# Kernel optimization log

Measured on AMD Instinct MI355X. Metric: run time of the kernel, lower is better.

Reference implementation:

```python
import jax, jax.numpy as jnp
import numpy as np

EPS = 1e-5

def _proj(x, w, b, gamma, beta, mean, var):
    # 1x1 conv (einsum over channels) + BatchNorm (inference) ; Dropout is identity in eval.
    y = jnp.einsum('bchw,oc->bohw', x, w) + b[None, :, None, None]
    scale = gamma * jax.lax.rsqrt(var + EPS)
    shift = beta - mean * scale
    return y * scale[None, :, None, None] + shift[None, :, None, None]

def _make_layer(key, cin, cout):
    k1, k2, k3, k4 = jax.random.split(key, 4)
    w = jax.random.normal(k1, (cout, cin), jnp.float32) * (1.0 / np.sqrt(cin))
    b = jax.random.normal(k2, (cout,), jnp.float32) * 0.01
    gamma = 1.0 + 0.1 * jax.random.normal(k3, (cout,), jnp.float32)
    beta = 0.1 * jax.random.normal(k4, (cout,), jnp.float32)
    mean = 0.05 * jax.random.normal(jax.random.fold_in(k1, 7), (cout,), jnp.float32)
    var = 0.5 + jax.random.uniform(jax.random.fold_in(k2, 7), (cout,), jnp.float32)
    return w, b, gamma, beta, mean, var

def setup_inputs() -> dict:
    key = jax.random.key(0)
    B, C, Ci, H, W = 4, 128, 64, 64, 64
    ks = jax.random.split(key, 6)
    inp = {
        'x1': jax.random.normal(ks[0], (B, C, H, W), jnp.float32),
        'x2': jax.random.normal(ks[1], (B, C, H, W), jnp.float32),
    }
    for name, k, cin, cout in [('theta', ks[2], C, Ci), ('phi', ks[3], C, Ci),
                               ('g', ks[4], C, Ci), ('wout', ks[5], Ci, C)]:
        w, b, gm, bt, mn, vr = _make_layer(k, cin, cout)
        inp.update({f'{name}_w': w, f'{name}_b': b, f'{name}_g': gm,
                    f'{name}_beta': bt, f'{name}_m': mn, f'{name}_v': vr})
    return inp

def reference(x1, x2,
              theta_w, theta_b, theta_g, theta_beta, theta_m, theta_v,
              phi_w, phi_b, phi_g, phi_beta, phi_m, phi_v,
              g_w, g_b, g_g, g_beta, g_m, g_v,
              wout_w, wout_b, wout_g, wout_beta, wout_m, wout_v):
    B, C, H, W = x1.shape
    N = H * W
    theta_x1 = _proj(x1, theta_w, theta_b, theta_g, theta_beta, theta_m, theta_v).reshape(B, -1, N)  # [B,Ci,N]
    phi_x2 = _proj(x2, phi_w, phi_b, phi_g, phi_beta, phi_m, phi_v).reshape(B, -1, N)                # [B,Ci,N]
    g_x2 = _proj(x2, g_w, g_b, g_g, g_beta, g_m, g_v).reshape(B, -1, N)                              # [B,Ci,N]
    # attention_map[b, n, m] = sum_c theta[b,c,n] * phi[b,c,m]
    attn = jax.nn.softmax(jnp.einsum('bcn,bcm->bnm', theta_x1, phi_x2), axis=-1)  # [B,N,N]
    out = jnp.einsum('bnm,bcm->bcn', attn, g_x2).reshape(B, -1, H, W)             # [B,Ci,H,W]
    out = _proj(out, wout_w, wout_b, wout_g, wout_beta, wout_m, wout_v)           # [B,C,H,W]
    return jnp.concatenate((out, x1), axis=1)                                     # [B,2C,H,W]
```

## Files before the change

### kernel.cpp

```cpp
#include <hip/hip_runtime.h>
#include <stdint.h>
#include <stddef.h>

#define EPS   1e-5f
#define CINCH 128
#define CI    64
#define NPIX  4096
#define KSPL  4
#define LOG2E 1.44269504088896340736f

typedef __bf16 bf16_t;
typedef _Float16 f16_t;
typedef bf16_t bf16x8 __attribute__((ext_vector_type(8)));
typedef f16_t  f16x8  __attribute__((ext_vector_type(8)));
typedef float  f32x4  __attribute__((ext_vector_type(4)));

typedef __attribute__((address_space(3))) unsigned int lds_u32;
typedef __attribute__((address_space(1))) const unsigned int glb_u32;

__device__ __forceinline__ f32x4 mfma16(bf16x8 a, bf16x8 b, f32x4 c) {
  return __builtin_amdgcn_mfma_f32_16x16x32_bf16(a, b, c, 0, 0, 0);
}
__device__ __forceinline__ f32x4 fzero4() {
  f32x4 z = {0.f, 0.f, 0.f, 0.f};
  return z;
}
__device__ __forceinline__ void gload16(const void* g, void* l) {
  __builtin_amdgcn_global_load_lds((glb_u32*)g, (lds_u32*)l, 16, 0, 0);
}


__global__ __launch_bounds__(256) void proj_all(
    const float* __restrict__ x1, const float* __restrict__ x2,
    const float* __restrict__ tw, const float* __restrict__ tb,
    const float* __restrict__ tg, const float* __restrict__ tbt,
    const float* __restrict__ tm, const float* __restrict__ tv,
    const float* __restrict__ pw, const float* __restrict__ pb,
    const float* __restrict__ pg, const float* __restrict__ pbt,
    const float* __restrict__ pm, const float* __restrict__ pv,
    const float* __restrict__ gw, const float* __restrict__ gb,
    const float* __restrict__ gg, const float* __restrict__ gbt,
    const float* __restrict__ gmn, const float* __restrict__ gv,
    bf16_t* __restrict__ thetaT_h, bf16_t* __restrict__ thetaT_l,
    bf16_t* __restrict__ phiT_h,   bf16_t* __restrict__ phiT_l,
    bf16_t* __restrict__ g_cm,     float* __restrict__ out)
{
  __shared__ float wT[CINCH][CI];
  __shared__ float bf[CI];
  __shared__ float xs[CINCH][32];
  __shared__ __align__(16) char tbuf[32 * 68 * 4];
  float (*tF)[68] = (float(*)[68])tbuf;
  float (*gT)[33] = (float(*)[33])tbuf;

  const int tid = threadIdx.x;
  const int b   = blockIdx.y;
  const int n0  = blockIdx.x * 32;
  const int px  = tid & 31;
  const int og  = tid >> 5;

  auto loadW = [&](const float* w, const float* bb_, const float* gm_,
                   const float* bt_, const float* mn_, const float* vr_,
                   float mul) {
    for (int idx = tid; idx < CI * CINCH; idx += 256) {
      const int o = idx & 63, c = idx >> 6;
      const float sc = gm_[o] * rsqrtf(vr_[o] + EPS);
      wT[c][o] = w[o * CINCH + c] * sc * mul;
      if (c == 0) bf[o] = (bb_[o] * sc + bt_[o] - mn_[o] * sc) * mul;
    }
  };
  auto stageX = [&](const float* x) {
    const float* xsrc = x + (size_t)b * CINCH * NPIX + n0;
#pragma unroll
    for (int i = 0; i < 4; ++i) {
      const int idx = i * 256 + tid;
      const int c = idx >> 3, p = idx & 7;
      *(f32x4*)&xs[c][p * 4] = *(const f32x4*)(xsrc + (size_t)c * NPIX + p * 4);
    }
  };
  auto compute = [&](float* acc) {
#pragma unroll
    for (int j = 0; j < 8; ++j) acc[j] = 0.f;
#pragma unroll 4
    for (int c0 = 0; c0 < CINCH; c0 += 4) {
      float xv[4];
#pragma unroll
      for (int cc = 0; cc < 4; ++cc) xv[cc] = xs[c0 + cc][px];
#pragma unroll
      for (int cc = 0; cc < 4; ++cc) {
        const f32x4 w0 = *(const f32x4*)&wT[c0 + cc][og * 8];
        const f32x4 w1 = *(const f32x4*)&wT[c0 + cc][og * 8 + 4];
#pragma unroll
        for (int j = 0; j < 4; ++j) {
          acc[j]     += w0[j] * xv[cc];
          acc[j + 4] += w1[j] * xv[cc];
        }
      }
    }
#pragma unroll
    for (int j = 0; j < 8; ++j) acc[j] += bf[og * 8 + j];
  };

  float acc[8];

  loadW(tw, tb, tg, tbt, tm, tv, LOG2E);
  {
    const float* xsrc = x1 + (size_t)b * CINCH * NPIX + n0;
    float* odst = out + ((size_t)b * 256 + 128) * NPIX + n0;
#pragma unroll
    for (int i = 0; i < 4; ++i) {
      const int idx = i * 256 + tid;
      const int c = idx >> 3, p = idx & 7;
      const f32x4 v = *(const f32x4*)(xsrc + (size_t)c * NPIX + p * 4);
      *(f32x4*)&xs[c][p * 4] = v;
      *(f32x4*)(odst + (size_t)c * NPIX + p * 4) = v;
    }
  }
  __syncthreads();
  compute(acc);
  __syncthreads();
#pragma unroll
  for (int j = 0; j < 8; ++j) tF[px][og * 8 + j] = acc[j];
  loadW(pw, pb, pg, pbt, pm, pv, 1.f);
  stageX(x2);
  __syncthreads();
  {
    const int px2 = tid >> 3, ogs = tid & 7;
    bf16x8 hv, lv;
#pragma unroll
    for (int j = 0; j < 8; ++j) {
      const float v = tF[px2][ogs * 8 + j];
      const bf16_t h = (bf16_t)v;
      hv[j] = h;
      lv[j] = (bf16_t)(v - (float)h);
    }
    const size_t base = ((size_t)b * NPIX + n0 + px2) * CI + ogs * 8;
    *(bf16x8*)(thetaT_h + base) = hv;
    *(bf16x8*)(thetaT_l + base) = lv;
  }

  compute(acc);
  __syncthreads();
#pragma unroll
  for (int j = 0; j < 8; ++j) tF[px][og * 8 + j] = acc[j];
  loadW(gw, gb, gg, gbt, gmn, gv, 1.f);
  __syncthreads();
  {
    const int px2 = tid >> 3, ogs = tid & 7;
    const int n = n0 + px2;
    bf16x8 hv, lv;
#pragma unroll
    for (int j = 0; j < 8; ++j) {
      const float v = tF[px2][ogs * 8 + j];
      const bf16_t h = (bf16_t)v;
      hv[j] = h;
      lv[j] = (bf16_t)(v - (float)h);
    }
    const size_t rowb = ((size_t)b * NPIX + n) * 128;
    const int byte = (ogs * 16) ^ ((n & 7) << 4);
    *(bf16x8*)((char*)phiT_h + rowb + byte) = hv;
    *(bf16x8*)((char*)phiT_l + rowb + byte) = lv;
  }

  compute(acc);
  __syncthreads();
#pragma unroll
  for (int j = 0; j < 8; ++j) gT[og * 8 + j][px] = acc[j];
  __syncthreads();
  {
    const int c = tid & 63, mgp = tid >> 6;
    bf16x8 gv;
#pragma unroll
    for (int j = 0; j < 8; ++j) gv[j] = (bf16_t)gT[c][mgp * 8 + j];
    *(bf16x8*)(g_cm + ((size_t)b * CI + c) * NPIX + n0 + mgp * 8) = gv;
  }
}

__global__ __launch_bounds__(256, 2) void flash_attn(
    const bf16_t* __restrict__ thetaT_h, const bf16_t* __restrict__ thetaT_l,
    const bf16_t* __restrict__ phiT_h,   const bf16_t* __restrict__ phiT_l,
    const bf16_t* __restrict__ g_cm,
    f16_t* __restrict__ Opart, float* __restrict__ mlbuf)
{
  __shared__ __attribute__((aligned(16))) char sT[2][24576];
  __shared__ __attribute__((aligned(16))) char sP[4][4096];

  const int tid  = threadIdx.x;
  const int lane = tid & 63;
  const int wid  = tid >> 6;
  const int lrow = lane & 15;
  const int lhi  = lane >> 4;

  const int wg = blockIdx.x;
  const int b  = wg >> 7;
  const int rr = wg & 127;
  const int qt = rr >> 2;
  const int ks = rr & 3;
  const int q0 = qt * 128 + wid * 32;
  const int t0 = ks * 16;

  const char* const srcPHb = (const char*)phiT_h + ((size_t)b * NPIX) * 128;
  const char* const srcPLb = (const char*)phiT_l + ((size_t)b * NPIX) * 128;
  const char* const srcVb  = (const char*)g_cm + (size_t)b * CI * NPIX * 2;

  auto stage = [&](int buf, int tile) {
    const size_t rb = (size_t)tile * 8192;
    char* const dst = sT[buf];
    gload16(srcPHb + rb + tid * 16,         dst + tid * 16);
    gload16(srcPHb + rb + (256 + tid) * 16, dst + (256 + tid) * 16);
    gload16(srcPLb + rb + tid * 16,         dst + 8192 + tid * 16);
    gload16(srcPLb + rb + (256 + tid) * 16, dst + 8192 + (256 + tid) * 16);
#pragma unroll
    for (int k = 0; k < 2; ++k) {
      const int c2 = k * 256 + tid;
      const int row = c2 >> 3, part = c2 & 7;
      gload16(srcVb + (size_t)row * (NPIX * 2) + tile * 128 +
                  ((part * 16) ^ ((row & 7) << 4)),
              dst + 16384 + c2 * 16);
    }
  };

  stage(0, t0);

  bf16x8 qh[2][2], qlv[2][2];
  {
    const bf16_t* qbh = thetaT_h + ((size_t)b * NPIX + q0 + lrow) * CI + lhi * 8;
    const bf16_t* qbl = thetaT_l + ((size_t)b * NPIX + q0 + lrow) * CI + lhi * 8;
#pragma unroll
    for (int nt = 0; nt < 2; ++nt)
#pragma unroll
      for (int kk = 0; kk < 2; ++kk) {
        qh[nt][kk]  = *(const bf16x8*)(qbh + nt * 16 * CI + kk * 32);
        qlv[nt][kk] = *(const bf16x8*)(qbl + nt * 16 * CI + kk * 32);
      }
  }

  f32x4 oacc[2][4];
#pragma unroll
  for (int a = 0; a < 2; ++a)
#pragma unroll
    for (int c = 0; c < 4; ++c) oacc[a][c] = fzero4();

  float m_run[2] = {-1e30f, -1e30f};
  float l_run[2] = {0.f, 0.f};

  char* const Pw = sP[wid];

  __syncthreads();

  for (int tt = 0; tt < 16; ++tt) {
    const int cur = tt & 1;
    if (tt < 15) stage(cur ^ 1, t0 + tt + 1);

    const char* const sKH = sT[cur];
    const char* const sKL = sT[cur] + 8192;
    const char* const sVc = sT[cur] + 16384;

    f32x4 s[4][2];
#pragma unroll
    for (int mt = 0; mt < 4; ++mt)
#pragma unroll
      for (int nt = 0; nt < 2; ++nt) s[mt][nt] = fzero4();

    __builtin_amdgcn_s_setprio(1);
#pragma unroll
    for (int mt = 0; mt < 4; ++mt) {
      const int row = mt * 16 + lrow;
      const int swz = (row & 7) << 4;
#pragma unroll
      for (int kk = 0; kk < 2; ++kk) {
        const int byte = row * 128 + ((kk * 64 + lhi * 16) ^ swz);
        const bf16x8 aH = *(const bf16x8*)(sKH + byte);
        const bf16x8 aL = *(const bf16x8*)(sKL + byte);
#pragma unroll
        for (int nt = 0; nt < 2; ++nt) {
          s[mt][nt] = mfma16(aH, qh[nt][kk],  s[mt][nt]);
          s[mt][nt] = mfma16(aH, qlv[nt][kk], s[mt][nt]);
          s[mt][nt] = mfma16(aL, qh[nt][kk],  s[mt][nt]);
        }
      }
    }
    __builtin_amdgcn_s_setprio(0);

    float mx[2], a2[2];
#pragma unroll
    for (int nt = 0; nt < 2; ++nt) {
      float m1 = fmaxf(fmaxf(s[0][nt][0], s[0][nt][1]), fmaxf(s[0][nt][2], s[0][nt][3]));
      float m2 = fmaxf(fmaxf(s[1][nt][0], s[1][nt][1]), fmaxf(s[1][nt][2], s[1][nt][3]));
      float m3 = fmaxf(fmaxf(s[2][nt][0], s[2][nt][1]), fmaxf(s[2][nt][2], s[2][nt][3]));
      float m4 = fmaxf(fmaxf(s[3][nt][0], s[3][nt][1]), fmaxf(s[3][nt][2], s[3][nt][3]));
      float m = fmaxf(fmaxf(m1, m2), fmaxf(m3, m4));
      m = fmaxf(m, __shfl_xor(m, 16));
      m = fmaxf(m, __shfl_xor(m, 32));
      mx[nt] = m;
    }
    const bool up = !__all((mx[0] <= m_run[0] + 5.f) && (mx[1] <= m_run[1] + 5.f));
#pragma unroll
    for (int nt = 0; nt < 2; ++nt) {
      const float mnew  = up ? fmaxf(m_run[nt], mx[nt]) : m_run[nt];
      const float alpha = up ? exp2f(m_run[nt] - mnew) : 1.f;
      float lsum = 0.f;
#pragma unroll
      for (int mt = 0; mt < 4; ++mt)
#pragma unroll
        for (int r = 0; r < 4; ++r) {
          const float p = exp2f(s[mt][nt][r] - mnew);
          s[mt][nt][r] = p;
          lsum += p;
        }
      lsum += __shfl_xor(lsum, 16);
      lsum += __shfl_xor(lsum, 32);
      l_run[nt] = l_run[nt] * alpha + lsum;
      m_run[nt] = mnew;
      a2[nt] = alpha;
    }

    if (up) {
#pragma unroll
      for (int qt2 = 0; qt2 < 2; ++qt2) {
#pragma unroll
        for (int r = 0; r < 4; ++r) {
          const float av = __shfl(a2[qt2], lhi * 4 + r);
#pragma unroll
          for (int ct = 0; ct < 4; ++ct) oacc[qt2][ct][r] *= av;
        }
      }
    }

#pragma unroll
    for (int mt = 0; mt < 4; ++mt)
#pragma unroll
      for (int nt = 0; nt < 2; ++nt) {
        union { bf16_t h[4]; uint32_t u[2]; } pk;
#pragma unroll
        for (int r = 0; r < 4; ++r) pk.h[r] = (bf16_t)s[mt][nt][r];
        const int q    = nt * 16 + lrow;
        const int mloc = mt * 16 + lhi * 4;
        const int byte = q * 128 + ((mloc * 2) ^ ((q & 7) << 4));
        *(uint2*)(Pw + byte) = make_uint2(pk.u[0], pk.u[1]);
      }

    bf16x8 bV[2][4];
#pragma unroll
    for (int ct = 0; ct < 4; ++ct) {
      const int row = ct * 16 + lrow;
      const int swz = (row & 7) << 4;
#pragma unroll
      for (int kk = 0; kk < 2; ++kk)
        bV[kk][ct] = *(const bf16x8*)(sVc + row * 128 + ((kk * 64 + lhi * 16) ^ swz));
    }
    __builtin_amdgcn_s_setprio(1);
#pragma unroll
    for (int qt2 = 0; qt2 < 2; ++qt2) {
      const int q = qt2 * 16 + lrow;
#pragma unroll
      for (int kk = 0; kk < 2; ++kk) {
        const bf16x8 pfrag =
            *(const bf16x8*)(Pw + q * 128 + ((kk * 64 + lhi * 16) ^ ((q & 7) << 4)));
#pragma unroll
        for (int ct = 0; ct < 4; ++ct)
          oacc[qt2][ct] = mfma16(pfrag, bV[kk][ct], oacc[qt2][ct]);
      }
    }
    __builtin_amdgcn_s_setprio(0);

    if (tt < 15) __syncthreads();
  }

  {
#pragma unroll
    for (int qt2 = 0; qt2 < 2; ++qt2)
#pragma unroll
      for (int ct = 0; ct < 4; ++ct)
#pragma unroll
        for (int r = 0; r < 4; ++r) {
          const int ql = qt2 * 16 + lhi * 4 + r;
          const int c  = ct * 16 + lrow;
          *(f16_t*)(Pw + (ql * 64 + c) * 2) = (f16_t)oacc[qt2][ct][r];
        }
    f16_t* const Ob = Opart + ((size_t)(b * KSPL + ks) * NPIX + q0) * 64;
#pragma unroll
    for (int i = 0; i < 4; ++i) {
      const int idx = i * 64 + lane;
      *(f16x8*)(Ob + idx * 8) = *(const f16x8*)(Pw + idx * 16);
    }
  }
  if (lhi < 2) {
    const int q = q0 + lhi * 16 + lrow;
    const size_t base = ((size_t)(b * KSPL + ks) * NPIX + q) * 2;
    mlbuf[base]     = m_run[lhi];
    mlbuf[base + 1] = l_run[lhi];
  }
}

__global__ __launch_bounds__(256) void merge_out(
    const f16_t* __restrict__ Opart, const float* __restrict__ mlbuf,
    const float* __restrict__ ww,  const float* __restrict__ wb,
    const float* __restrict__ wg,  const float* __restrict__ wbt,
    const float* __restrict__ wm,  const float* __restrict__ wvv,
    float* __restrict__ out)
{
  __shared__ float wlds[128][64];
  __shared__ float bfw[128];
  __shared__ float mrg[32][68];

  const int tid = threadIdx.x;
  const int b   = blockIdx.y;
  const int n0  = blockIdx.x * 32;

  for (int idx = tid; idx < 128 * 64; idx += 256) {
    const int o = idx >> 6, c = idx & 63;
    const float sc = wg[o] * rsqrtf(wvv[o] + EPS);
    wlds[o][c] = ww[o * 64 + c] * sc;
    if (c == 0) bfw[o] = wb[o] * sc + wbt[o] - wm[o] * sc;
  }

  {
    const int px = tid & 31;
    const int cg = tid >> 5;
    const int q  = n0 + px;
    float mk[KSPL], lk[KSPL];
#pragma unroll
    for (int ks = 0; ks < KSPL; ++ks) {
      const size_t base = ((size_t)(b * KSPL + ks) * NPIX + q) * 2;
      mk[ks] = mlbuf[base];
      lk[ks] = mlbuf[base + 1];
    }
    float M = mk[0];
#pragma unroll
    for (int ks = 1; ks < KSPL; ++ks) M = fmaxf(M, mk[ks]);
    float al[KSPL]; float den = 0.f;
#pragma unroll
    for (int ks = 0; ks < KSPL; ++ks) { al[ks] = exp2f(mk[ks] - M); den += al[ks] * lk[ks]; }
    const float inv = 1.f / den;
#pragma unroll
    for (int ks = 0; ks < KSPL; ++ks) al[ks] *= inv;

    float r[8];
#pragma unroll
    for (int j = 0; j < 8; ++j) r[j] = 0.f;
#pragma unroll
    for (int ks = 0; ks < KSPL; ++ks) {
      const f16x8 p = *(const f16x8*)(Opart +
          ((size_t)(b * KSPL + ks) * NPIX + q) * 64 + cg * 8);
#pragma unroll
      for (int j = 0; j < 8; ++j) r[j] += (float)p[j] * al[ks];
    }
#pragma unroll
    for (int j = 0; j < 8; ++j) mrg[px][cg * 8 + j] = r[j];
  }
  __syncthreads();

  const int px = tid & 31;
  const int oh = tid >> 5;
  float acc[16];
#pragma unroll
  for (int j = 0; j < 16; ++j) acc[j] = 0.f;

#pragma unroll 4
  for (int c0 = 0; c0 < 64; c0 += 4) {
    const f32x4 m4 = *(const f32x4*)&mrg[px][c0];
#pragma unroll
    for (int j = 0; j < 16; ++j) {
      const f32x4 w4 = *(const f32x4*)&wlds[oh * 16 + j][c0];
      acc[j] += w4[0] * m4[0] + w4[1] * m4[1] + w4[2] * m4[2] + w4[3] * m4[3];
    }
  }
#pragma unroll
  for (int j = 0; j < 16; ++j) {
    const int o = oh * 16 + j;
    out[((size_t)b * 256 + o) * NPIX + n0 + px] = acc[j] + bfw[o];
  }
}

extern "C" void kernel_launch(void* const* d_in, const int* in_sizes, int n_in,
                              void* d_out, int out_size, void* d_ws, size_t ws_size,
                              hipStream_t stream) {
  (void)in_sizes; (void)n_in; (void)out_size; (void)ws_size;
  const float* x1  = (const float*)d_in[0];
  const float* x2  = (const float*)d_in[1];
  const float* tw  = (const float*)d_in[2];
  const float* tb  = (const float*)d_in[3];
  const float* tg  = (const float*)d_in[4];
  const float* tbt = (const float*)d_in[5];
  const float* tm  = (const float*)d_in[6];
  const float* tv  = (const float*)d_in[7];
  const float* pw  = (const float*)d_in[8];
  const float* pb  = (const float*)d_in[9];
  const float* pg  = (const float*)d_in[10];
  const float* pbt = (const float*)d_in[11];
  const float* pm  = (const float*)d_in[12];
  const float* pv  = (const float*)d_in[13];
  const float* gw  = (const float*)d_in[14];
  const float* gb  = (const float*)d_in[15];
  const float* gg  = (const float*)d_in[16];
  const float* gbt = (const float*)d_in[17];
  const float* gmn = (const float*)d_in[18];
  const float* gv  = (const float*)d_in[19];
  const float* ww  = (const float*)d_in[20];
  const float* wb  = (const float*)d_in[21];
  const float* wg  = (const float*)d_in[22];
  const float* wbt = (const float*)d_in[23];
  const float* wm  = (const float*)d_in[24];
  const float* wv  = (const float*)d_in[25];

  float* out = (float*)d_out;
  char*  ws  = (char*)d_ws;
  bf16_t* thetaT_h = (bf16_t*)(ws);
  bf16_t* thetaT_l = (bf16_t*)(ws + (size_t)(2)  * 1048576);
  bf16_t* phiT_h   = (bf16_t*)(ws + (size_t)(4)  * 1048576);
  bf16_t* phiT_l   = (bf16_t*)(ws + (size_t)(6)  * 1048576);
  bf16_t* g_cm     = (bf16_t*)(ws + (size_t)(8)  * 1048576);
  f16_t*  Opart    = (f16_t*) (ws + (size_t)(10) * 1048576);
  float*  mlbuf    = (float*) (ws + (size_t)(18) * 1048576);

  dim3 gp(128, 4);
  proj_all<<<gp, 256, 0, stream>>>(x1, x2,
                                   tw, tb, tg, tbt, tm, tv,
                                   pw, pb, pg, pbt, pm, pv,
                                   gw, gb, gg, gbt, gmn, gv,
                                   thetaT_h, thetaT_l, phiT_h, phiT_l,
                                   g_cm, out);
  flash_attn<<<512, 256, 0, stream>>>(thetaT_h, thetaT_l, phiT_h, phiT_l,
                                      g_cm, Opart, mlbuf);
  merge_out<<<gp, 256, 0, stream>>>(Opart, mlbuf, ww, wb, wg, wbt, wm, wv, out);
}
```

Measured before the change: 226.6 us.

## Load K/V fragments directly from global memory and raise split-K to six

Removes the double-buffered LDS staging of phi/g tiles in the flash-attention kernel. Each wave now reads its MFMA operands straight from global memory (relying on L2), which drops the per-tile block barrier and frees LDS so the occupancy hint can rise to three blocks per CU. The key split grows from four to six parts, giving a grid of 768 blocks, and the phi store drops its swizzle to match the new unswizzled reads. The cost is redundant global/L2 traffic, since every wave fetches the same K/V tile, and uneven 10/11-tile splits. The merge kernel must also handle six partials.

```diff
diff --git a/kernel.cpp b/kernel.cpp
--- a/kernel.cpp
+++ b/kernel.cpp
@@ -6,7 +6,7 @@
 #define CINCH 128
 #define CI    64
 #define NPIX  4096
-#define KSPL  4
+#define KSPL  6
 #define LOG2E 1.44269504088896340736f
 
 typedef __bf16 bf16_t;
@@ -15,18 +15,12 @@
 typedef f16_t  f16x8  __attribute__((ext_vector_type(8)));
 typedef float  f32x4  __attribute__((ext_vector_type(4)));
 
-typedef __attribute__((address_space(3))) unsigned int lds_u32;
-typedef __attribute__((address_space(1))) const unsigned int glb_u32;
-
 __device__ __forceinline__ f32x4 mfma16(bf16x8 a, bf16x8 b, f32x4 c) {
   return __builtin_amdgcn_mfma_f32_16x16x32_bf16(a, b, c, 0, 0, 0);
 }
 __device__ __forceinline__ f32x4 fzero4() {
   f32x4 z = {0.f, 0.f, 0.f, 0.f};
   return z;
-}
-__device__ __forceinline__ void gload16(const void* g, void* l) {
-  __builtin_amdgcn_global_load_lds((glb_u32*)g, (lds_u32*)l, 16, 0, 0);
 }
 
 
@@ -99,6 +93,20 @@
 #pragma unroll
     for (int j = 0; j < 8; ++j) acc[j] += bf[og * 8 + j];
   };
+  auto storeHL = [&](bf16_t* dh, bf16_t* dl) {
+    const int px2 = tid >> 3, ogs = tid & 7;
+    bf16x8 hv, lv;
+#pragma unroll
+    for (int j = 0; j < 8; ++j) {
+      const float v = tF[px2][ogs * 8 + j];
+      const bf16_t h = (bf16_t)v;
+      hv[j] = h;
+      lv[j] = (bf16_t)(v - (float)h);
+    }
+    const size_t base = ((size_t)b * NPIX + n0 + px2) * CI + ogs * 8;
+    *(bf16x8*)(dh + base) = hv;
+    *(bf16x8*)(dl + base) = lv;
+  };
 
   float acc[8];
 
@@ -123,20 +131,7 @@
   loadW(pw, pb, pg, pbt, pm, pv, 1.f);
   stageX(x2);
   __syncthreads();
-  {
-    const int px2 = tid >> 3, ogs = tid & 7;
-    bf16x8 hv, lv;
-#pragma unroll
-    for (int j = 0; j < 8; ++j) {
-      const float v = tF[px2][ogs * 8 + j];
-      const bf16_t h = (bf16_t)v;
-      hv[j] = h;
-      lv[j] = (bf16_t)(v - (float)h);
-    }
-    const size_t base = ((size_t)b * NPIX + n0 + px2) * CI + ogs * 8;
-    *(bf16x8*)(thetaT_h + base) = hv;
-    *(bf16x8*)(thetaT_l + base) = lv;
-  }
+  storeHL(thetaT_h, thetaT_l);
 
   compute(acc);
   __syncthreads();
@@ -144,22 +139,7 @@
   for (int j = 0; j < 8; ++j) tF[px][og * 8 + j] = acc[j];
   loadW(gw, gb, gg, gbt, gmn, gv, 1.f);
   __syncthreads();
-  {
-    const int px2 = tid >> 3, ogs = tid & 7;
-    const int n = n0 + px2;
-    bf16x8 hv, lv;
-#pragma unroll
-    for (int j = 0; j < 8; ++j) {
-      const float v = tF[px2][ogs * 8 + j];
-      const bf16_t h = (bf16_t)v;
-      hv[j] = h;
-      lv[j] = (bf16_t)(v - (float)h);
-    }
-    const size_t rowb = ((size_t)b * NPIX + n) * 128;
-    const int byte = (ogs * 16) ^ ((n & 7) << 4);
-    *(bf16x8*)((char*)phiT_h + rowb + byte) = hv;
-    *(bf16x8*)((char*)phiT_l + rowb + byte) = lv;
-  }
+  storeHL(phiT_h, phiT_l);
 
   compute(acc);
   __syncthreads();
@@ -168,20 +148,19 @@
   __syncthreads();
   {
     const int c = tid & 63, mgp = tid >> 6;
-    bf16x8 gv;
-#pragma unroll
-    for (int j = 0; j < 8; ++j) gv[j] = (bf16_t)gT[c][mgp * 8 + j];
-    *(bf16x8*)(g_cm + ((size_t)b * CI + c) * NPIX + n0 + mgp * 8) = gv;
-  }
-}
-
-__global__ __launch_bounds__(256, 2) void flash_attn(
+    bf16x8 gvv;
+#pragma unroll
+    for (int j = 0; j < 8; ++j) gvv[j] = (bf16_t)gT[c][mgp * 8 + j];
+    *(bf16x8*)(g_cm + ((size_t)b * CI + c) * NPIX + n0 + mgp * 8) = gvv;
+  }
+}
+
+__global__ __launch_bounds__(256, 3) void flash_attn(
     const bf16_t* __restrict__ thetaT_h, const bf16_t* __restrict__ thetaT_l,
     const bf16_t* __restrict__ phiT_h,   const bf16_t* __restrict__ phiT_l,
     const bf16_t* __restrict__ g_cm,
     f16_t* __restrict__ Opart, float* __restrict__ mlbuf)
 {
-  __shared__ __attribute__((aligned(16))) char sT[2][24576];
   __shared__ __attribute__((aligned(16))) char sP[4][4096];
 
   const int tid  = threadIdx.x;
@@ -191,35 +170,17 @@
   const int lhi  = lane >> 4;
 
   const int wg = blockIdx.x;
-  const int b  = wg >> 7;
-  const int rr = wg & 127;
-  const int qt = rr >> 2;
-  const int ks = rr & 3;
+  const int b  = wg / 192;
+  const int rr = wg % 192;
+  const int qt = rr / KSPL;
+  const int ks = rr % KSPL;
   const int q0 = qt * 128 + wid * 32;
-  const int t0 = ks * 16;
-
-  const char* const srcPHb = (const char*)phiT_h + ((size_t)b * NPIX) * 128;
-  const char* const srcPLb = (const char*)phiT_l + ((size_t)b * NPIX) * 128;
-  const char* const srcVb  = (const char*)g_cm + (size_t)b * CI * NPIX * 2;
-
-  auto stage = [&](int buf, int tile) {
-    const size_t rb = (size_t)tile * 8192;
-    char* const dst = sT[buf];
-    gload16(srcPHb + rb + tid * 16,         dst + tid * 16);
-    gload16(srcPHb + rb + (256 + tid) * 16, dst + (256 + tid) * 16);
-    gload16(srcPLb + rb + tid * 16,         dst + 8192 + tid * 16);
-    gload16(srcPLb + rb + (256 + tid) * 16, dst + 8192 + (256 + tid) * 16);
-#pragma unroll
-    for (int k = 0; k < 2; ++k) {
-      const int c2 = k * 256 + tid;
-      const int row = c2 >> 3, part = c2 & 7;
-      gload16(srcVb + (size_t)row * (NPIX * 2) + tile * 128 +
-                  ((part * 16) ^ ((row & 7) << 4)),
-              dst + 16384 + c2 * 16);
-    }
-  };
-
-  stage(0, t0);
+  const int t0 = (ks * 64) / KSPL;
+  const int t1 = ((ks + 1) * 64) / KSPL;
+
+  const bf16_t* const phH = phiT_h + ((size_t)b * NPIX + lrow) * CI + lhi * 8;
+  const bf16_t* const phL = phiT_l + ((size_t)b * NPIX + lrow) * CI + lhi * 8;
+  const bf16_t* const gvb = g_cm + ((size_t)b * CI + lrow) * NPIX + lhi * 8;
 
   bf16x8 qh[2][2], qlv[2][2];
   {
@@ -245,15 +206,8 @@
 
   char* const Pw = sP[wid];
 
-  __syncthreads();
-
-  for (int tt = 0; tt < 16; ++tt) {
-    const int cur = tt & 1;
-    if (tt < 15) stage(cur ^ 1, t0 + tt + 1);
-
-    const char* const sKH = sT[cur];
-    const char* const sKL = sT[cur] + 8192;
-    const char* const sVc = sT[cur] + 16384;
+  for (int t = t0; t < t1; ++t) {
+    const int key0 = t * 64;
 
     f32x4 s[4][2];
 #pragma unroll
@@ -261,25 +215,33 @@
 #pragma unroll
       for (int nt = 0; nt < 2; ++nt) s[mt][nt] = fzero4();
 
-    __builtin_amdgcn_s_setprio(1);
 #pragma unroll
     for (int mt = 0; mt < 4; ++mt) {
-      const int row = mt * 16 + lrow;
-      const int swz = (row & 7) << 4;
-#pragma unroll
-      for (int kk = 0; kk < 2; ++kk) {
-        const int byte = row * 128 + ((kk * 64 + lhi * 16) ^ swz);
-        const bf16x8 aH = *(const bf16x8*)(sKH + byte);
-        const bf16x8 aL = *(const bf16x8*)(sKL + byte);
-#pragma unroll
-        for (int nt = 0; nt < 2; ++nt) {
-          s[mt][nt] = mfma16(aH, qh[nt][kk],  s[mt][nt]);
-          s[mt][nt] = mfma16(aH, qlv[nt][kk], s[mt][nt]);
-          s[mt][nt] = mfma16(aL, qh[nt][kk],  s[mt][nt]);
-        }
-      }
-    }
-    __builtin_amdgcn_s_setprio(0);
+      const size_t roff = (size_t)(key0 + mt * 16) * CI;
+      bf16x8 aH0 = *(const bf16x8*)(phH + roff);
+      bf16x8 aH1 = *(const bf16x8*)(phH + roff + 32);
+      bf16x8 aL0 = *(const bf16x8*)(phL + roff);
+      bf16x8 aL1 = *(const bf16x8*)(phL + roff + 32);
+      __builtin_amdgcn_s_setprio(1);
+#pragma unroll
+      for (int nt = 0; nt < 2; ++nt) {
+        s[mt][nt] = mfma16(aH0, qh[nt][0],  s[mt][nt]);
+        s[mt][nt] = mfma16(aH0, qlv[nt][0], s[mt][nt]);
+        s[mt][nt] = mfma16(aL0, qh[nt][0],  s[mt][nt]);
+        s[mt][nt] = mfma16(aH1, qh[nt][1],  s[mt][nt]);
+        s[mt][nt] = mfma16(aH1, qlv[nt][1], s[mt][nt]);
+        s[mt][nt] = mfma16(aL1, qh[nt][1],  s[mt][nt]);
+      }
+      __builtin_amdgcn_s_setprio(0);
+    }
+
+    bf16x8 bV[2][4];
+#pragma unroll
+    for (int ct = 0; ct < 4; ++ct)
+#pragma unroll
+      for (int kk = 0; kk < 2; ++kk)
+        bV[kk][ct] = *(const bf16x8*)(gvb + (size_t)ct * 16 * NPIX +
+                                      key0 + kk * 32);
 
     float mx[2], a2[2];
 #pragma unroll
@@ -339,15 +301,6 @@
         *(uint2*)(Pw + byte) = make_uint2(pk.u[0], pk.u[1]);
       }
 
-    bf16x8 bV[2][4];
-#pragma unroll
-    for (int ct = 0; ct < 4; ++ct) {
-      const int row = ct * 16 + lrow;
-      const int swz = (row & 7) << 4;
-#pragma unroll
-      for (int kk = 0; kk < 2; ++kk)
-        bV[kk][ct] = *(const bf16x8*)(sVc + row * 128 + ((kk * 64 + lhi * 16) ^ swz));
-    }
     __builtin_amdgcn_s_setprio(1);
 #pragma unroll
     for (int qt2 = 0; qt2 < 2; ++qt2) {
@@ -362,8 +315,6 @@
       }
     }
     __builtin_amdgcn_s_setprio(0);
-
-    if (tt < 15) __syncthreads();
   }
 
   {
@@ -511,7 +462,7 @@
   bf16_t* phiT_l   = (bf16_t*)(ws + (size_t)(6)  * 1048576);
   bf16_t* g_cm     = (bf16_t*)(ws + (size_t)(8)  * 1048576);
   f16_t*  Opart    = (f16_t*) (ws + (size_t)(10) * 1048576);
-  float*  mlbuf    = (float*) (ws + (size_t)(18) * 1048576);
+  float*  mlbuf    = (float*) (ws + (size_t)(23) * 1048576);
 
   dim3 gp(128, 4);
   proj_all<<<gp, 256, 0, stream>>>(x1, x2,
@@ -520,7 +471,7 @@
                                    gw, gb, gg, gbt, gmn, gv,
                                    thetaT_h, thetaT_l, phiT_h, phiT_l,
                                    g_cm, out);
-  flash_attn<<<512, 256, 0, stream>>>(thetaT_h, thetaT_l, phiT_h, phiT_l,
+  flash_attn<<<768, 256, 0, stream>>>(thetaT_h, thetaT_l, phiT_h, phiT_l,
                                       g_cm, Opart, mlbuf);
   merge_out<<<gp, 256, 0, stream>>>(Opart, mlbuf, ww, wb, wg, wbt, wm, wv, out);
 }
```

Result: slower. 266.2 us (+17.5%).
